# Kernel optimization log

Measured on AMD Instinct MI355X. Metric: run time of the kernel, lower is better.

The kernel has to match this reference:

```python
import jax, jax.numpy as jnp
import numpy as np

N_NODES = 50000
N_EDGES = 100000
NODE_IN = 64
EDGE_IN = 16
H = 32          # node_hidden_feats
EDGE_HID = 128  # edge_hidden_feats
STEPS = 6       # num_step_message_passing


def setup_inputs() -> dict:
    key = jax.random.key(0)
    ks = jax.random.split(key, 12)
    s = lambda k, *sh: jax.random.normal(k, sh, dtype=jnp.float32) * 0.05
    return {
        "node_ids": jax.random.randint(ks[0], (N_NODES,), 0, 343),
        "edge_ids": jax.random.randint(ks[1], (N_EDGES,), 0, 21),
        "src": jax.random.randint(ks[2], (N_EDGES,), 0, N_NODES),
        "dst": jax.random.randint(ks[3], (N_EDGES,), 0, N_NODES),
        "node_emb": s(ks[4], 343, NODE_IN),
        "edge_emb": s(ks[5], 21, EDGE_IN),
        "proj_W": s(ks[6], NODE_IN, H),
        "proj_b": jnp.zeros((H,), jnp.float32),
        "eW1": s(ks[7], EDGE_IN, EDGE_HID),
        "eb1": jnp.zeros((EDGE_HID,), jnp.float32),
        "eW2": s(ks[8], EDGE_HID, H * H),
        "eb2": jnp.zeros((H * H,), jnp.float32),
        "conv_bias": jnp.zeros((H,), jnp.float32),
        "gru_Wih": s(ks[9], 3 * H, H),
        "gru_Whh": s(ks[10], 3 * H, H),
        "gru_bih": jnp.zeros((3 * H,), jnp.float32),
        "gru_bhh": jnp.zeros((3 * H,), jnp.float32),
    }


def reference(node_ids, edge_ids, src, dst, node_emb, edge_emb, proj_W, proj_b,
              eW1, eb1, eW2, eb2, conv_bias, gru_Wih, gru_Whh, gru_bih, gru_bhh):
    # project node features
    h = jax.nn.relu(node_emb[node_ids] @ proj_W + proj_b)                 # [N, H]
    e = edge_emb[edge_ids]                                                # [E, EDGE_IN]
    # edge-conditioned weight matrices (edge feats are fixed, so identical every step)
    W_e = (jax.nn.relu(e @ eW1 + eb1) @ eW2 + eb2).reshape(N_EDGES, H, H)  # [E, H, H]
    hidden = h
    for _ in range(STEPS):
        # NNConv: gather src feats, per-edge matvec, scatter-sum to dst, + bias
        msg = jnp.einsum('ei,eio->eo', h[src], W_e)                        # [E, H]
        agg = jax.ops.segment_sum(msg, dst, num_segments=N_NODES) + conv_bias
        m = jax.nn.relu(agg)
        # GRU cell (PyTorch gate order: r, z, n)
        gi = m @ gru_Wih.T + gru_bih                                       # [N, 3H]
        gh = hidden @ gru_Whh.T + gru_bhh                                  # [N, 3H]
        ir, iz, inew = jnp.split(gi, 3, axis=-1)
        hr, hz, hnew = jnp.split(gh, 3, axis=-1)
        r = jax.nn.sigmoid(ir + hr)
        z = jax.nn.sigmoid(iz + hz)
        n = jnp.tanh(inew + r * hnew)
        hidden = (1.0 - z) * n + z * hidden
        h = hidden
    return h
```

## Files before the change

### kernel.cpp

```cpp
#include <hip/hip_runtime.h>

#define N_NODES 50000
#define N_EDGES 100000
#define NT 21
#define STEPS 6
#define BPT 40
#define NB 100
#define EPB 1000

__device__ __forceinline__ float sigm(float x) { return 1.f / (1.f + __expf(-x)); }
__device__ __forceinline__ float tanh_f(float x) {
    float t = __expf(2.f * fabsf(x));
    return copysignf(1.f - 2.f / (t + 1.f), x);
}

__global__ __launch_bounds__(256) void k_proj(const int* __restrict__ node_ids,
                                              const float* __restrict__ node_emb,
                                              const float* __restrict__ W,
                                              const float* __restrict__ b,
                                              float* __restrict__ h) {
    int lane = threadIdx.x & 31;
    int n = blockIdx.x * 8 + (threadIdx.x >> 5);
    if (n >= N_NODES) return;
    float w[64];
#pragma unroll
    for (int i = 0; i < 64; ++i) w[i] = W[i * 32 + lane];
    int id = node_ids[n];
    const float* er = node_emb + id * 64;
    float e0 = er[lane];
    float e1 = er[32 + lane];
    float acc = b[lane];
#pragma unroll
    for (int i = 0; i < 32; ++i) acc += __shfl(e0, i, 32) * w[i];
#pragma unroll
    for (int i = 0; i < 32; ++i) acc += __shfl(e1, i, 32) * w[32 + i];
    h[n * 32 + lane] = fmaxf(acc, 0.f);
}

__global__ __launch_bounds__(128) void k_wtable(const float* __restrict__ edge_emb,
                                                const float* __restrict__ eW1,
                                                const float* __restrict__ eb1,
                                                const float* __restrict__ eW2,
                                                const float* __restrict__ eb2,
                                                float* __restrict__ Wt) {
    __shared__ float x[128];
    int t = blockIdx.x >> 3, c = blockIdx.x & 7;
    int tid = threadIdx.x;
    float acc = eb1[tid];
#pragma unroll
    for (int i = 0; i < 16; ++i) acc += edge_emb[t * 16 + i] * eW1[i * 128 + tid];
    x[tid] = fmaxf(acc, 0.f);
    __syncthreads();
    int j = c * 128 + tid;
    float a = eb2[j];
#pragma unroll 8
    for (int i = 0; i < 128; ++i) a += x[i] * eW2[i * 1024 + j];
    Wt[t * 1024 + j] = a;
}

__global__ __launch_bounds__(256) void k_hist(const int* __restrict__ eid,
                                              int* __restrict__ hist) {
    __shared__ int lc[NT];
    if (threadIdx.x < NT) lc[threadIdx.x] = 0;
    __syncthreads();
    int e0 = blockIdx.x * EPB;
#pragma unroll
    for (int k = 0; k < EPB / 256 + 1; ++k) {
        int e = e0 + k * 256 + threadIdx.x;
        if (e < e0 + EPB) atomicAdd(&lc[eid[e]], 1);
    }
    __syncthreads();
    if (threadIdx.x < NT) hist[blockIdx.x * NT + threadIdx.x] = lc[threadIdx.x];
}

__global__ void k_offs(const int* __restrict__ hist,
                       int* __restrict__ offs,
                       int* __restrict__ cnt,
                       int* __restrict__ base) {
    __shared__ int tot[NT];
    int t = threadIdx.x;
    if (t < NT) {
        int run = 0;
        for (int b = 0; b < NB; ++b) { offs[b * NT + t] = run; run += hist[b * NT + t]; }
        tot[t] = run;
        cnt[t] = run;
    }
    __syncthreads();
    if (t == 0) {
        int r = 0;
        for (int tt = 0; tt < NT; ++tt) { base[tt] = r; r += tot[tt]; }
    }
}

__global__ __launch_bounds__(256) void k_fill2(const int* __restrict__ eid,
                                               const int* __restrict__ offs,
                                               const int* __restrict__ base,
                                               int* __restrict__ perm) {
    __shared__ int cur[NT];
    int b = blockIdx.x;
    if (threadIdx.x < NT) cur[threadIdx.x] = base[threadIdx.x] + offs[b * NT + threadIdx.x];
    __syncthreads();
    int e0 = b * EPB;
#pragma unroll
    for (int k = 0; k < EPB / 256 + 1; ++k) {
        int e = e0 + k * 256 + threadIdx.x;
        if (e < e0 + EPB) {
            int r = atomicAdd(&cur[eid[e]], 1);
            perm[r] = e;
        }
    }
}

__global__ __launch_bounds__(256) void k_msg(const int* __restrict__ perm,
                                             const int* __restrict__ base,
                                             const int* __restrict__ cnt,
                                             const int* __restrict__ src,
                                             const int* __restrict__ dst,
                                             const float* __restrict__ Wt,
                                             const float* __restrict__ h,
                                             float* __restrict__ agg) {
    int t = blockIdx.x / BPT, sub = blockIdx.x % BPT;
    int lane = threadIdx.x & 31, g = threadIdx.x >> 5;
    const float* wp = Wt + t * 1024;
    float w[32];
#pragma unroll
    for (int i = 0; i < 32; ++i) w[i] = wp[i * 32 + lane];
    int n = cnt[t], b0 = base[t];
    for (int idx = sub * 8 + g; idx < n; idx += BPT * 8) {
        int e = perm[b0 + idx];
        int s = src[e], d = dst[e];
        float hv = h[s * 32 + lane];
        float acc = 0.f;
#pragma unroll
        for (int i = 0; i < 32; ++i) acc += __shfl(hv, i, 32) * w[i];
        atomicAdd(&agg[d * 32 + lane], acc);
    }
}

__global__ __launch_bounds__(256) void k_gru(const float* __restrict__ Wih,
                                             const float* __restrict__ Whh,
                                             const float* __restrict__ bih,
                                             const float* __restrict__ bhh,
                                             const float* __restrict__ cb,
                                             float* __restrict__ agg,
                                             float* __restrict__ h) {
    __shared__ float wiT[32 * 96];
    __shared__ float whT[32 * 96];
    int t = threadIdx.x;
#pragma unroll
    for (int kk = 0; kk < 3; ++kk)
#pragma unroll
        for (int it = 0; it < 4; ++it) {
            int k = (t & 31) + 32 * kk;
            int i = (t >> 5) + 8 * it;
            wiT[i * 96 + k] = Wih[k * 32 + i];
            whT[i * 96 + k] = Whh[k * 32 + i];
        }
    __syncthreads();

    int gtid = blockIdx.x * 256 + t;
    int p = gtid >> 3;
    if (p >= N_NODES / 2) return;
    int j = gtid & 7, kb = j * 4;

    float* a0 = agg + (size_t)(2 * p) * 32;
    float* a1 = a0 + 32;
    float* h0p = h + (size_t)(2 * p) * 32;
    float* h1p = h0p + 32;

    float accR0[4] = {0, 0, 0, 0}, accR1[4] = {0, 0, 0, 0};
    float accZ0[4] = {0, 0, 0, 0}, accZ1[4] = {0, 0, 0, 0};
    float accI0[4] = {0, 0, 0, 0}, accI1[4] = {0, 0, 0, 0};
    float accH0[4] = {0, 0, 0, 0}, accH1[4] = {0, 0, 0, 0};

#pragma unroll
    for (int c = 0; c < 8; ++c) {
        float4 cb4 = ((const float4*)cb)[c];
        float4 ma = ((const float4*)a0)[c];
        float4 mb = ((const float4*)a1)[c];
        float4 ha = ((const float4*)h0p)[c];
        float4 hb = ((const float4*)h1p)[c];
        float m0[4] = {fmaxf(ma.x + cb4.x, 0.f), fmaxf(ma.y + cb4.y, 0.f),
                       fmaxf(ma.z + cb4.z, 0.f), fmaxf(ma.w + cb4.w, 0.f)};
        float m1[4] = {fmaxf(mb.x + cb4.x, 0.f), fmaxf(mb.y + cb4.y, 0.f),
                       fmaxf(mb.z + cb4.z, 0.f), fmaxf(mb.w + cb4.w, 0.f)};
        float h0v[4] = {ha.x, ha.y, ha.z, ha.w};
        float h1v[4] = {hb.x, hb.y, hb.z, hb.w};
#pragma unroll
        for (int e = 0; e < 4; ++e) {
            int i = 4 * c + e;
            const float* wb = wiT + i * 96 + kb;
            const float* vb = whT + i * 96 + kb;
            float4 wiR = *(const float4*)(wb);
            float4 whR = *(const float4*)(vb);
            float4 wiZ = *(const float4*)(wb + 32);
            float4 whZ = *(const float4*)(vb + 32);
            float4 wiN = *(const float4*)(wb + 64);
            float4 whN = *(const float4*)(vb + 64);
            float mi0 = m0[e], mi1 = m1[e], hi0 = h0v[e], hi1 = h1v[e];
            accR0[0] += mi0 * wiR.x + hi0 * whR.x;
            accR0[1] += mi0 * wiR.y + hi0 * whR.y;
            accR0[2] += mi0 * wiR.z + hi0 * whR.z;
            accR0[3] += mi0 * wiR.w + hi0 * whR.w;
            accR1[0] += mi1 * wiR.x + hi1 * whR.x;
            accR1[1] += mi1 * wiR.y + hi1 * whR.y;
            accR1[2] += mi1 * wiR.z + hi1 * whR.z;
            accR1[3] += mi1 * wiR.w + hi1 * whR.w;
            accZ0[0] += mi0 * wiZ.x + hi0 * whZ.x;
            accZ0[1] += mi0 * wiZ.y + hi0 * whZ.y;
            accZ0[2] += mi0 * wiZ.z + hi0 * whZ.z;
            accZ0[3] += mi0 * wiZ.w + hi0 * whZ.w;
            accZ1[0] += mi1 * wiZ.x + hi1 * whZ.x;
            accZ1[1] += mi1 * wiZ.y + hi1 * whZ.y;
            accZ1[2] += mi1 * wiZ.z + hi1 * whZ.z;
            accZ1[3] += mi1 * wiZ.w + hi1 * whZ.w;
            accI0[0] += mi0 * wiN.x;  accH0[0] += hi0 * whN.x;
            accI0[1] += mi0 * wiN.y;  accH0[1] += hi0 * whN.y;
            accI0[2] += mi0 * wiN.z;  accH0[2] += hi0 * whN.z;
            accI0[3] += mi0 * wiN.w;  accH0[3] += hi0 * whN.w;
            accI1[0] += mi1 * wiN.x;  accH1[0] += hi1 * whN.x;
            accI1[1] += mi1 * wiN.y;  accH1[1] += hi1 * whN.y;
            accI1[2] += mi1 * wiN.z;  accH1[2] += hi1 * whN.z;
            accI1[3] += mi1 * wiN.w;  accH1[3] += hi1 * whN.w;
        }
    }

    float4 hv0 = ((const float4*)h0p)[j];
    float4 hv1 = ((const float4*)h1p)[j];
    float hs0[4] = {hv0.x, hv0.y, hv0.z, hv0.w};
    float hs1[4] = {hv1.x, hv1.y, hv1.z, hv1.w};

    float out0[4], out1[4];
#pragma unroll
    for (int q = 0; q < 4; ++q) {
        float bR = bih[kb + q] + bhh[kb + q];
        float bZ = bih[32 + kb + q] + bhh[32 + kb + q];
        float biN = bih[64 + kb + q];
        float bhN = bhh[64 + kb + q];
        float r0 = sigm(accR0[q] + bR);
        float z0 = sigm(accZ0[q] + bZ);
        float n0 = tanh_f(accI0[q] + biN + r0 * (accH0[q] + bhN));
        out0[q] = (1.f - z0) * n0 + z0 * hs0[q];
        float r1 = sigm(accR1[q] + bR);
        float z1 = sigm(accZ1[q] + bZ);
        float n1 = tanh_f(accI1[q] + biN + r1 * (accH1[q] + bhN));
        out1[q] = (1.f - z1) * n1 + z1 * hs1[q];
    }

    float4 z4 = make_float4(0.f, 0.f, 0.f, 0.f);
    ((float4*)a0)[j] = z4;
    ((float4*)a1)[j] = z4;
    ((float4*)h0p)[j] = make_float4(out0[0], out0[1], out0[2], out0[3]);
    ((float4*)h1p)[j] = make_float4(out1[0], out1[1], out1[2], out1[3]);
}

extern "C" void kernel_launch(void* const* d_in, const int* in_sizes, int n_in,
                              void* d_out, int out_size, void* d_ws, size_t ws_size,
                              hipStream_t stream) {
    const int*   node_ids  = (const int*)d_in[0];
    const int*   edge_ids  = (const int*)d_in[1];
    const int*   src       = (const int*)d_in[2];
    const int*   dst       = (const int*)d_in[3];
    const float* node_emb  = (const float*)d_in[4];
    const float* edge_emb  = (const float*)d_in[5];
    const float* proj_W    = (const float*)d_in[6];
    const float* proj_b    = (const float*)d_in[7];
    const float* eW1       = (const float*)d_in[8];
    const float* eb1       = (const float*)d_in[9];
    const float* eW2       = (const float*)d_in[10];
    const float* eb2       = (const float*)d_in[11];
    const float* conv_bias = (const float*)d_in[12];
    const float* gWih      = (const float*)d_in[13];
    const float* gWhh      = (const float*)d_in[14];
    const float* gbih      = (const float*)d_in[15];
    const float* gbhh      = (const float*)d_in[16];

    float* h = (float*)d_out;
    char* ws = (char*)d_ws;
    float* agg  = (float*)ws;
    float* Wt   = (float*)(ws + 6400 * 1024);
    int*   hist = (int*)(ws + 6400 * 1024 + 128 * 1024);
    int*   offs = hist + NB * NT;
    int*   cnt  = offs + NB * NT;
    int*   base = cnt + 32;
    int*   perm = base + 32;

    hipMemsetAsync(agg, 0, (size_t)N_NODES * 32 * sizeof(float), stream);

    k_proj<<<(N_NODES + 7) / 8, 256, 0, stream>>>(node_ids, node_emb, proj_W, proj_b, h);
    k_wtable<<<NT * 8, 128, 0, stream>>>(edge_emb, eW1, eb1, eW2, eb2, Wt);
    k_hist<<<NB, 256, 0, stream>>>(edge_ids, hist);
    k_offs<<<1, 64, 0, stream>>>(hist, offs, cnt, base);
    k_fill2<<<NB, 256, 0, stream>>>(edge_ids, offs, base, perm);

    for (int s = 0; s < STEPS; ++s) {
        k_msg<<<NT * BPT, 256, 0, stream>>>(perm, base, cnt, src, dst, Wt, h, agg);
        k_gru<<<(N_NODES / 2 * 8 + 255) / 256, 256, 0, stream>>>(gWih, gWhh, gbih, gbhh, conv_bias, agg, h);
    }
}
```

Baseline: 488.2 us.

## Prefetch edges in message kernel and pre-transpose GRU weights once

The message kernel now software-pipelines its edge loop: it loads the index, src and dst of the edge two iterations ahead and the source feature row one iteration ahead, so gather latency overlaps the per-edge matvec. Blocks per edge type are doubled. GRU weights are transposed once into workspace by a new small kernel, which removes the per-block shared-memory staging and barrier; the GRU kernel then reads those weights from global memory (cache) instead of LDS. The GRU kernel also double-buffers its agg/h row loads in registers and reuses them for the final state blend. The risks are higher register pressure and slower weight reads from cache than from LDS.

```diff
diff --git a/kernel.cpp b/kernel.cpp
--- a/kernel.cpp
+++ b/kernel.cpp
@@ -4,7 +4,7 @@
 #define N_EDGES 100000
 #define NT 21
 #define STEPS 6
-#define BPT 40
+#define BPT 80
 #define NB 100
 #define EPB 1000
 
@@ -56,6 +56,16 @@
 #pragma unroll 8
     for (int i = 0; i < 128; ++i) a += x[i] * eW2[i * 1024 + j];
     Wt[t * 1024 + j] = a;
+}
+
+__global__ void k_tr(const float* __restrict__ Wih, const float* __restrict__ Whh,
+                     float* __restrict__ WTih, float* __restrict__ WThh) {
+    int u = blockIdx.x * 256 + threadIdx.x;
+    if (u < 3072) {
+        int k = u >> 5, i = u & 31;
+        WTih[i * 96 + k] = Wih[u];
+        WThh[i * 96 + k] = Whh[u];
+    }
 }
 
 __global__ __launch_bounds__(256) void k_hist(const int* __restrict__ eid,
@@ -126,39 +136,40 @@
 #pragma unroll
     for (int i = 0; i < 32; ++i) w[i] = wp[i * 32 + lane];
     int n = cnt[t], b0 = base[t];
-    for (int idx = sub * 8 + g; idx < n; idx += BPT * 8) {
-        int e = perm[b0 + idx];
-        int s = src[e], d = dst[e];
-        float hv = h[s * 32 + lane];
+    const int stride = BPT * 8;
+    int idx = sub * 8 + g;
+
+    bool v0 = idx < n, v1 = (idx + stride) < n;
+    int s0 = 0, d0 = 0, s1 = 0, d1 = 0;
+    if (v0) { int e = perm[b0 + idx]; s0 = src[e]; d0 = dst[e]; }
+    if (v1) { int e = perm[b0 + idx + stride]; s1 = src[e]; d1 = dst[e]; }
+    float hv = v0 ? h[s0 * 32 + lane] : 0.f;
+    int nextIdx = idx + 2 * stride;
+
+    while (v0) {
+        float hvN = 0.f;
+        if (v1) hvN = h[s1 * 32 + lane];
+        int s2 = 0, d2 = 0;
+        bool v2 = nextIdx < n;
+        if (v2) { int e = perm[b0 + nextIdx]; s2 = src[e]; d2 = dst[e]; }
         float acc = 0.f;
 #pragma unroll
         for (int i = 0; i < 32; ++i) acc += __shfl(hv, i, 32) * w[i];
-        atomicAdd(&agg[d * 32 + lane], acc);
-    }
-}
-
-__global__ __launch_bounds__(256) void k_gru(const float* __restrict__ Wih,
-                                             const float* __restrict__ Whh,
+        atomicAdd(&agg[d0 * 32 + lane], acc);
+        s0 = s1; d0 = d1; v0 = v1; hv = hvN;
+        s1 = s2; d1 = d2; v1 = v2;
+        nextIdx += stride;
+    }
+}
+
+__global__ __launch_bounds__(256) void k_gru(const float* __restrict__ WTih,
+                                             const float* __restrict__ WThh,
                                              const float* __restrict__ bih,
                                              const float* __restrict__ bhh,
                                              const float* __restrict__ cb,
                                              float* __restrict__ agg,
                                              float* __restrict__ h) {
-    __shared__ float wiT[32 * 96];
-    __shared__ float whT[32 * 96];
-    int t = threadIdx.x;
-#pragma unroll
-    for (int kk = 0; kk < 3; ++kk)
-#pragma unroll
-        for (int it = 0; it < 4; ++it) {
-            int k = (t & 31) + 32 * kk;
-            int i = (t >> 5) + 8 * it;
-            wiT[i * 96 + k] = Wih[k * 32 + i];
-            whT[i * 96 + k] = Whh[k * 32 + i];
-        }
-    __syncthreads();
-
-    int gtid = blockIdx.x * 256 + t;
+    int gtid = blockIdx.x * 256 + threadIdx.x;
     int p = gtid >> 3;
     if (p >= N_NODES / 2) return;
     int j = gtid & 7, kb = j * 4;
@@ -173,13 +184,27 @@
     float accI0[4] = {0, 0, 0, 0}, accI1[4] = {0, 0, 0, 0};
     float accH0[4] = {0, 0, 0, 0}, accH1[4] = {0, 0, 0, 0};
 
+    float4 hs0f = make_float4(0.f, 0.f, 0.f, 0.f);
+    float4 hs1f = make_float4(0.f, 0.f, 0.f, 0.f);
+
+    float4 bufA[2], bufB[2], bufC[2], bufD[2];
+    bufA[0] = ((const float4*)a0)[0];
+    bufB[0] = ((const float4*)a1)[0];
+    bufC[0] = ((const float4*)h0p)[0];
+    bufD[0] = ((const float4*)h1p)[0];
+
 #pragma unroll
     for (int c = 0; c < 8; ++c) {
+        const int cur = c & 1, nxt = cur ^ 1;
+        if (c < 7) {
+            bufA[nxt] = ((const float4*)a0)[c + 1];
+            bufB[nxt] = ((const float4*)a1)[c + 1];
+            bufC[nxt] = ((const float4*)h0p)[c + 1];
+            bufD[nxt] = ((const float4*)h1p)[c + 1];
+        }
+        float4 ma = bufA[cur], mb = bufB[cur], ha = bufC[cur], hb = bufD[cur];
+        if (c == j) { hs0f = ha; hs1f = hb; }
         float4 cb4 = ((const float4*)cb)[c];
-        float4 ma = ((const float4*)a0)[c];
-        float4 mb = ((const float4*)a1)[c];
-        float4 ha = ((const float4*)h0p)[c];
-        float4 hb = ((const float4*)h1p)[c];
         float m0[4] = {fmaxf(ma.x + cb4.x, 0.f), fmaxf(ma.y + cb4.y, 0.f),
                        fmaxf(ma.z + cb4.z, 0.f), fmaxf(ma.w + cb4.w, 0.f)};
         float m1[4] = {fmaxf(mb.x + cb4.x, 0.f), fmaxf(mb.y + cb4.y, 0.f),
@@ -189,8 +214,8 @@
 #pragma unroll
         for (int e = 0; e < 4; ++e) {
             int i = 4 * c + e;
-            const float* wb = wiT + i * 96 + kb;
-            const float* vb = whT + i * 96 + kb;
+            const float* wb = WTih + i * 96 + kb;
+            const float* vb = WThh + i * 96 + kb;
             float4 wiR = *(const float4*)(wb);
             float4 whR = *(const float4*)(vb);
             float4 wiZ = *(const float4*)(wb + 32);
@@ -225,10 +250,8 @@
         }
     }
 
-    float4 hv0 = ((const float4*)h0p)[j];
-    float4 hv1 = ((const float4*)h1p)[j];
-    float hs0[4] = {hv0.x, hv0.y, hv0.z, hv0.w};
-    float hs1[4] = {hv1.x, hv1.y, hv1.z, hv1.w};
+    float hs0[4] = {hs0f.x, hs0f.y, hs0f.z, hs0f.w};
+    float hs1[4] = {hs1f.x, hs1f.y, hs1f.z, hs1f.w};
 
     float out0[4], out1[4];
 #pragma unroll
@@ -279,6 +302,8 @@
     char* ws = (char*)d_ws;
     float* agg  = (float*)ws;
     float* Wt   = (float*)(ws + 6400 * 1024);
+    float* WTih = (float*)(ws + 6400 * 1024 + 96 * 1024);
+    float* WThh = (float*)(ws + 6400 * 1024 + 96 * 1024 + 12 * 1024);
     int*   hist = (int*)(ws + 6400 * 1024 + 128 * 1024);
     int*   offs = hist + NB * NT;
     int*   cnt  = offs + NB * NT;
@@ -289,12 +314,13 @@
 
     k_proj<<<(N_NODES + 7) / 8, 256, 0, stream>>>(node_ids, node_emb, proj_W, proj_b, h);
     k_wtable<<<NT * 8, 128, 0, stream>>>(edge_emb, eW1, eb1, eW2, eb2, Wt);
+    k_tr<<<12, 256, 0, stream>>>(gWih, gWhh, WTih, WThh);
     k_hist<<<NB, 256, 0, stream>>>(edge_ids, hist);
     k_offs<<<1, 64, 0, stream>>>(hist, offs, cnt, base);
     k_fill2<<<NB, 256, 0, stream>>>(edge_ids, offs, base, perm);
 
     for (int s = 0; s < STEPS; ++s) {
         k_msg<<<NT * BPT, 256, 0, stream>>>(perm, base, cnt, src, dst, Wt, h, agg);
-        k_gru<<<(N_NODES / 2 * 8 + 255) / 256, 256, 0, stream>>>(gWih, gWhh, gbih, gbhh, conv_bias, agg, h);
-    }
-}
+        k_gru<<<(N_NODES / 2 * 8 + 255) / 256, 256, 0, stream>>>(WTih, WThh, gbih, gbhh, conv_bias, agg, h);
+    }
+}
```

Measured after the change: 1.401 ms. 187% more time.
